# Performance work log

Measured on AMD Instinct MI355X. Metric: run time of the kernel, lower is better.

Reference implementation:

```python
import jax, jax.numpy as jnp
import numpy as np

KS, PH, PW, SH, SW = 3, 1, 1, 1, 1


def setup_inputs() -> dict:
    key = jax.random.key(0)
    k1, k2, k3 = jax.random.split(key, 3)
    bs, p_in, H, W = 8, 64, 64, 64
    p_out = 64
    vs = KS * KS + 1
    x = jax.random.normal(k1, (bs, p_in, H, W), dtype=jnp.float32)
    # kaiming-uniform-like init scale for filters (fan_in = p_in*vs*vs)
    fan_in = p_in * vs * vs
    bound = float(np.sqrt(6.0 / fan_in))
    filters = jax.random.uniform(k2, (p_out, p_in, vs, vs), dtype=jnp.float32,
                                 minval=-bound, maxval=bound)
    biases = jax.random.uniform(k3, (p_out,), dtype=jnp.float32, minval=-1.0, maxval=1.0)
    return {"x": x, "filters": filters, "biases": biases}


def reference(x, filters, biases):
    # x: (bs, p_in, H, W); filters: (p_out, p_in, vs, vs); biases: (p_out,)
    bs, p_in = x.shape[0], x.shape[1]
    p_out = filters.shape[0]
    vs = KS * KS + 1
    # Extract ks x ks patches -> (bs, p_in*ks*ks, Ho, Wo), feature dim ordered (C, kh, kw)
    patches = jax.lax.conv_general_dilated_patches(
        x, filter_shape=(KS, KS), window_strides=(SH, SW),
        padding=[(PH, PH), (PW, PW)])
    Ho, Wo = patches.shape[-2], patches.shape[-1]
    P = patches.reshape(bs, p_in, KS * KS, Ho, Wo)
    # Prepend constant 1 -> augmented patch vector s of length vs (matches torch cat(ones, spot))
    ones = jnp.ones((bs, p_in, 1, Ho, Wo), dtype=x.dtype)
    S = jnp.concatenate([ones, P], axis=2)            # (bs, p_in, vs, Ho, Wo)
    # Move pixels to a single leading dim: (M, p_in, vs) with M = bs*Ho*Wo
    S = S.transpose(0, 3, 4, 1, 2).reshape(bs * Ho * Wo, p_in, vs)
    # Per-pixel, per-channel outer product s s^T: (M, p_in, vs, vs)
    Q = S[:, :, :, None] * S[:, :, None, :]
    # Quadratic form contraction with filters as one GEMM:
    # out[m, o] = sum_{c,i,j} Q[m,c,i,j] * filters[o,c,i,j]
    out = Q.reshape(bs * Ho * Wo, p_in * vs * vs) @ filters.reshape(p_out, -1).T
    out = out + biases[None, :]
    return out.reshape(bs, Ho, Wo, p_out).transpose(0, 3, 1, 2)
```

## Files before the change

kernel.cpp:

```cpp
#include <hip/hip_runtime.h>
#include <stdint.h>

#define HH 64
#define WW 64
#define PIN 64
#define POUT 64
#define NFEAT 54

typedef _Float16 half8 __attribute__((ext_vector_type(8)));
typedef _Float16 half4 __attribute__((ext_vector_type(4)));
typedef float f32x4 __attribute__((ext_vector_type(4)));
typedef float f32x16 __attribute__((ext_vector_type(16)));

__device__ constexpr int KT[54] = {0,0,0,0,0,0,0,0,0, 1,1,1,1,1,1,1,1,1, 2,2,2,2,2,2,2,2,
                                   3,3,3,3,3,3,3, 4,4,4,4,4,4, 5,5,5,5,5, 6,6,6,6, 7,7,7, 8,8, 9};
__device__ constexpr int LT[54] = {1,2,3,4,5,6,7,8,9, 1,2,3,4,5,6,7,8,9, 2,3,4,5,6,7,8,9,
                                   3,4,5,6,7,8,9, 4,5,6,7,8,9, 5,6,7,8,9, 6,7,8,9, 7,8,9, 8,9, 9};

__global__ void prep_filters(const float* __restrict__ f, const float* __restrict__ bias,
                             _Float16* __restrict__ fprep, float* __restrict__ fconst) {
    if (blockIdx.x == 108) {
        int o = threadIdx.x;
        if (o < POUT) {
            float s = bias[o];
            for (int c = 0; c < PIN; ++c) s += f[(size_t)(o * PIN + c) * 100];
            fconst[o] = s;
        }
        return;
    }
    int tid = blockIdx.x * 256 + threadIdx.x;
    int feat = tid >> 9;
    int rem = tid & 511;
    int o = rem >> 3;
    int cg = rem & 7;
    int k = KT[feat], l = LT[feat];

    half8 chunk;
    #pragma unroll
    for (int jj = 0; jj < 8; ++jj) {
        int c = cg * 8 + jj;
        const float* fc = f + (size_t)(o * PIN + c) * 100;
        float v;
        if (k == 0)      v = fc[l] + fc[l * 10];
        else if (k == l) v = fc[k * 10 + k];
        else             v = fc[k * 10 + l] + fc[l * 10 + k];
        chunk[jj] = (_Float16)v;
    }
    int lane = (o & 31) + 32 * (cg & 1);
    size_t byte = (size_t)feat * 8192 + (cg >> 1) * 2048 + (o >> 5) * 1024 + lane * 16;
    *(half8*)((char*)fprep + byte) = chunk;
}

__global__ __launch_bounds__(512, 4) void poly2d_mfma(
    const float* __restrict__ x, const _Float16* __restrict__ fprep,
    const float* __restrict__ fconst, float* __restrict__ out)
{
    __shared__ __align__(16) char smx[25344];

    const int t = threadIdx.x;
    const int lane = t & 63;
    const int wid = t >> 6;
    const int bid = (blockIdx.x & 7) * 64 + (blockIdx.x >> 3);
    const int b = bid >> 6;
    const int hrow = bid & 63;

    {
        const int w = t & 63;
        const int wl = w + 1;
        #pragma unroll
        for (int h = 0; h < 3; ++h) {
            int h_in = hrow - 1 + h;
            bool hok = ((unsigned)h_in < HH);
            #pragma unroll
            for (int cc = 0; cc < 2; ++cc) {
                int c = wid * 8 + cc * 4;
                float v0 = 0.f, v1 = 0.f, v2 = 0.f, v3 = 0.f;
                if (hok) {
                    const float* gx = x + (((size_t)b * PIN + c) * HH + h_in) * WW + w;
                    v0 = gx[0]; v1 = gx[4096]; v2 = gx[8192]; v3 = gx[12288];
                }
                half4 pk = {(_Float16)v0, (_Float16)v1, (_Float16)v2, (_Float16)v3};
                int byte = ((h * 66 + wl) * 8 + ((c >> 3) ^ (wl & 7))) * 16 + (c & 7) * 2;
                *(half4*)(smx + byte) = pk;
            }
        }
        if (t < 48) {
            int h = t >> 4, side = (t >> 3) & 1, cg = t & 7;
            int wl2 = side ? 65 : 0;
            int byte = ((h * 66 + wl2) * 8 + (cg ^ (wl2 & 7))) * 16;
            f32x4 z = {0.f, 0.f, 0.f, 0.f};
            *(f32x4*)(smx + byte) = z;
        }
    }
    __syncthreads();

    const int kc = wid >> 1;
    const int mwid = wid & 1;
    const int wbase = mwid * 32;
    const int l31 = lane & 31;
    const int lhi = lane >> 5;

    half8 xp[9];
    #pragma unroll
    for (int p = 1; p <= 9; ++p) {
        const int dh = (p - 1) / 3 - 1, dw = (p - 1) % 3 - 1;
        int wl = wbase + l31 + dw + 1;
        int hidx = dh + 1;
        int cgl = kc * 2 + lhi;
        int byte = ((hidx * 66 + wl) * 8 + (cgl ^ (wl & 7))) * 16;
        xp[p - 1] = *(const half8*)(smx + byte);
    }
    __syncthreads();

    const char* fbase = (const char*)fprep + (kc << 11) + (lane << 4);

    half8 Bb[3][2];
    #pragma unroll
    for (int s = 0; s < 2; ++s) {
        Bb[s][0] = *(const half8*)(fbase + (size_t)s * 8192);
        Bb[s][1] = *(const half8*)(fbase + (size_t)s * 8192 + 1024);
    }

    f32x16 acc0 = {}, acc1 = {};

    #pragma unroll
    for (int f = 0; f < NFEAT; ++f) {
        if (f + 2 < NFEAT) {
            Bb[(f + 2) % 3][0] = *(const half8*)(fbase + (size_t)(f + 2) * 8192);
            Bb[(f + 2) % 3][1] = *(const half8*)(fbase + (size_t)(f + 2) * 8192 + 1024);
        }
        constexpr_loop_body: ;
        const int k = KT[f], l = LT[f];
        half8 a = (k == 0) ? xp[l - 1] : xp[k - 1] * xp[l - 1];
        acc0 = __builtin_amdgcn_mfma_f32_32x32x16_f16(a, Bb[f % 3][0], acc0, 0, 0, 0);
        acc1 = __builtin_amdgcn_mfma_f32_32x32x16_f16(a, Bb[f % 3][1], acc1, 0, 0, 0);
    }

    __syncthreads();
    float* os = (float*)smx;

    #pragma unroll
    for (int pass = 0; pass < 4; ++pass) {
        if (kc == pass) {
            #pragma unroll
            for (int nb = 0; nb < 2; ++nb) {
                #pragma unroll
                for (int r = 0; r < 16; ++r) {
                    int row = (r & 3) + 8 * (r >> 2) + 4 * lhi;
                    int m = mwid * 32 + row;
                    int col = l31 + nb * 32;
                    float v = nb ? acc1[r] : acc0[r];
                    if (pass == 0) os[m * 65 + col] = v;
                    else           os[m * 65 + col] += v;
                }
            }
        }
        __syncthreads();
    }

    {
        const int w = t & 63;
        #pragma unroll
        for (int oo = 0; oo < 8; ++oo) {
            int o = wid * 8 + oo;
            float val = os[w * 65 + o] + fconst[o];
            out[(((size_t)b * POUT + o) * HH + hrow) * WW + w] = val;
        }
    }
}

__global__ __launch_bounds__(256) void poly2d_fp32(
    const float* __restrict__ x, const float* __restrict__ f,
    const float* __restrict__ bias, float* __restrict__ out)
{
    const int t = threadIdx.x;
    const int wo = t & 63;
    const int ho = (blockIdx.x & 15) * 4 + (t >> 6);
    const int o = (blockIdx.x >> 4) & 63;
    const int b = blockIdx.x >> 10;

    float acc = bias[o];
    const float* xb = x + (size_t)b * PIN * HH * WW;
    const float* fo = f + (size_t)o * PIN * 100;
    for (int c = 0; c < PIN; ++c) {
        const float* xc = xb + (size_t)c * HH * WW;
        float s[10];
        s[0] = 1.0f;
        #pragma unroll
        for (int kh = 0; kh < 3; ++kh) {
            int h = ho - 1 + kh;
            bool hok = ((unsigned)h < HH);
            #pragma unroll
            for (int kw = 0; kw < 3; ++kw) {
                int w = wo - 1 + kw;
                s[1 + kh * 3 + kw] = (hok && (unsigned)w < WW) ? xc[h * WW + w] : 0.0f;
            }
        }
        const float* fc = fo + c * 100;
        #pragma unroll
        for (int i = 0; i < 10; ++i) {
            float wsum = 0.0f;
            #pragma unroll
            for (int j = 0; j < 10; ++j) wsum = fmaf(fc[i * 10 + j], s[j], wsum);
            acc = fmaf(wsum, s[i], acc);
        }
    }
    out[(((size_t)b * POUT + o) * HH + ho) * WW + wo] = acc;
}

extern "C" void kernel_launch(void* const* d_in, const int* in_sizes, int n_in,
                              void* d_out, int out_size, void* d_ws, size_t ws_size,
                              hipStream_t stream) {
    const float* x    = (const float*)d_in[0];
    const float* filt = (const float*)d_in[1];
    const float* bias = (const float*)d_in[2];
    float* out = (float*)d_out;

    const size_t FPREP_BYTES = (size_t)NFEAT * POUT * PIN * 2;
    if (ws_size < FPREP_BYTES + 256) {
        poly2d_fp32<<<dim3(8 * 64 * 16), dim3(256), 0, stream>>>(x, filt, bias, out);
        return;
    }
    _Float16* fprep = (_Float16*)d_ws;
    float* fconst = (float*)((char*)d_ws + FPREP_BYTES);

    prep_filters<<<dim3(109), dim3(256), 0, stream>>>(filt, bias, fprep, fconst);
    poly2d_mfma<<<dim3(512), dim3(512), 0, stream>>>(x, fprep, fconst, out);
}
```

Before: 29.84 us.

## Stage filter tiles into LDS with async global_load_lds double buffering

Filter fragments used to be read straight from global memory into registers by every wave, which duplicated reads across the four M-waves and tied each read to the MFMA loop. They are now copied in 3-feature segments into a double-buffered LDS region with global_load_lds, using explicit vmcnt waits and barriers, and each wave reads its fragments from LDS. This cuts duplicated global/L2 traffic and overlaps the next copy with compute. In exchange it adds 48KB of LDS per block, which may lower occupancy against launch_bounds(512,4), and two block-wide barriers per segment.

```diff
diff --git a/kernel.cpp b/kernel.cpp
--- a/kernel.cpp
+++ b/kernel.cpp
@@ -6,6 +6,8 @@
 #define PIN 64
 #define POUT 64
 #define NFEAT 54
+#define SEGB 24576
+#define NSEG 18
 
 typedef _Float16 half8 __attribute__((ext_vector_type(8)));
 typedef _Float16 half4 __attribute__((ext_vector_type(4)));
@@ -55,6 +57,7 @@
     const float* __restrict__ x, const _Float16* __restrict__ fprep,
     const float* __restrict__ fconst, float* __restrict__ out)
 {
+    __shared__ __align__(16) char smB[2 * SEGB];
     __shared__ __align__(16) char smx[25344];
 
     const int t = threadIdx.x;
@@ -63,6 +66,20 @@
     const int bid = (blockIdx.x & 7) * 64 + (blockIdx.x >> 3);
     const int b = bid >> 6;
     const int hrow = bid & 63;
+
+#define STAGE(ss)                                                                         \
+    do {                                                                                  \
+        const char* s_ = (const char*)fprep + (size_t)(ss) * SEGB;                        \
+        _Pragma("unroll")                                                                 \
+        for (int r_ = 0; r_ < 3; ++r_)                                                    \
+            __builtin_amdgcn_global_load_lds(                                             \
+                (const __attribute__((address_space(1))) unsigned int*)(const void*)(s_ + r_ * 8192 + t * 16), \
+                (__attribute__((address_space(3))) unsigned int*)(void*)(smB + ((ss) & 1) * SEGB + r_ * 8192 + (wid << 10)), \
+                16, 0, 0);                                                                \
+    } while (0)
+
+    STAGE(0);
+    STAGE(1);
 
     {
         const int w = t & 63;
@@ -112,29 +129,39 @@
     }
     __syncthreads();
 
-    const char* fbase = (const char*)fprep + (kc << 11) + (lane << 4);
-
-    half8 Bb[3][2];
-    #pragma unroll
-    for (int s = 0; s < 2; ++s) {
-        Bb[s][0] = *(const half8*)(fbase + (size_t)s * 8192);
-        Bb[s][1] = *(const half8*)(fbase + (size_t)s * 8192 + 1024);
-    }
-
     f32x16 acc0 = {}, acc1 = {};
 
     #pragma unroll
-    for (int f = 0; f < NFEAT; ++f) {
-        if (f + 2 < NFEAT) {
-            Bb[(f + 2) % 3][0] = *(const half8*)(fbase + (size_t)(f + 2) * 8192);
-            Bb[(f + 2) % 3][1] = *(const half8*)(fbase + (size_t)(f + 2) * 8192 + 1024);
-        }
-        constexpr_loop_body: ;
-        const int k = KT[f], l = LT[f];
-        half8 a = (k == 0) ? xp[l - 1] : xp[k - 1] * xp[l - 1];
-        acc0 = __builtin_amdgcn_mfma_f32_32x32x16_f16(a, Bb[f % 3][0], acc0, 0, 0, 0);
-        acc1 = __builtin_amdgcn_mfma_f32_32x32x16_f16(a, Bb[f % 3][1], acc1, 0, 0, 0);
-    }
+    for (int s = 0; s < NSEG; ++s) {
+        if (s == NSEG - 1) { asm volatile("s_waitcnt vmcnt(0)" ::: "memory"); }
+        else               { asm volatile("s_waitcnt vmcnt(3)" ::: "memory"); }
+        asm volatile("" ::: "memory");
+        __builtin_amdgcn_s_barrier();
+        asm volatile("" ::: "memory");
+
+        const char* bseg = smB + (s & 1) * SEGB + (kc << 11) + (lane << 4);
+        half8 Bb0[3], Bb1[3];
+        #pragma unroll
+        for (int j = 0; j < 3; ++j) {
+            Bb0[j] = *(const half8*)(bseg + j * 8192);
+            Bb1[j] = *(const half8*)(bseg + j * 8192 + 1024);
+        }
+        #pragma unroll
+        for (int j = 0; j < 3; ++j) {
+            const int f = s * 3 + j;
+            const int k = KT[f], l = LT[f];
+            half8 a = (k == 0) ? xp[l - 1] : xp[k - 1] * xp[l - 1];
+            acc0 = __builtin_amdgcn_mfma_f32_32x32x16_f16(a, Bb0[j], acc0, 0, 0, 0);
+            acc1 = __builtin_amdgcn_mfma_f32_32x32x16_f16(a, Bb1[j], acc1, 0, 0, 0);
+        }
+
+        asm volatile("s_waitcnt lgkmcnt(0)" ::: "memory");
+        asm volatile("" ::: "memory");
+        __builtin_amdgcn_s_barrier();
+        asm volatile("" ::: "memory");
+        if (s + 2 < NSEG) STAGE(s + 2);
+    }
+#undef STAGE
 
     __syncthreads();
     float* os = (float*)smx;
```

Result: faster. 29.23 us (-2.0%).
